# Kernel optimization log

Hardware: AMD Instinct MI355X
Metric: run time of the kernel (lower is better)

The kernel has to match this reference:

```python
import jax, jax.numpy as jnp
import numpy as np

EMB = 512
N_ROWS = 10000
N_PAIRS = 65536


def setup_inputs() -> dict:
    key = jax.random.key(0)
    ks = jax.random.split(key, 10)
    s1 = 1.0 / np.sqrt(2 * EMB)
    s2 = 1.0 / np.sqrt(128)
    s3 = 1.0 / np.sqrt(64)
    return {
        "pos_pairs": jax.random.randint(ks[0], (N_PAIRS, 3), 0, N_ROWS, dtype=jnp.int32),
        "neg_pairs": jax.random.randint(ks[1], (N_PAIRS, 3), 0, N_ROWS, dtype=jnp.int32),
        "drug_embedding": jax.random.normal(ks[2], (N_ROWS, EMB), dtype=jnp.float32),
        "target_embedding": jax.random.normal(ks[3], (N_ROWS, EMB), dtype=jnp.float32),
        "W1": jax.random.normal(ks[4], (2 * EMB, 128), dtype=jnp.float32) * s1,
        "b1": jnp.zeros((128,), dtype=jnp.float32),
        "W2": jax.random.normal(ks[5], (128, 64), dtype=jnp.float32) * s2,
        "b2": jnp.zeros((64,), dtype=jnp.float32),
        "W3": jax.random.normal(ks[6], (64, 1), dtype=jnp.float32) * s3,
        "b3": jnp.zeros((1,), dtype=jnp.float32),
    }


def _mlp(x, W1, b1, W2, b2, W3, b3):
    h = jax.nn.relu(x @ W1 + b1)
    h = jax.nn.relu(h @ W2 + b2)
    return (h @ W3 + b3)[..., 0]  # [N]


def _pair_loss(pairs, drug_emb, tgt_emb, W1, b1, W2, b2, W3, b3):
    d = drug_emb[pairs[:, 0]]            # [N, EMB]
    t1 = tgt_emb[pairs[:, 1]]            # [N, EMB]
    t2 = tgt_emb[pairs[:, 2]]            # [N, EMB]
    a1 = _mlp(jnp.concatenate([d, t1], axis=-1), W1, b1, W2, b2, W3, b3)
    a2 = _mlp(jnp.concatenate([d, t2], axis=-1), W1, b1, W2, b2, W3, b3)
    # per-pair MSE of scalar affinities = (a1 - a2)^2; mean over pairs
    return jnp.mean((a1 - a2) ** 2)


def reference(pos_pairs, neg_pairs, drug_embedding, target_embedding,
              W1, b1, W2, b2, W3, b3):
    pos = _pair_loss(pos_pairs, drug_embedding, target_embedding, W1, b1, W2, b2, W3, b3)
    neg = _pair_loss(neg_pairs, drug_embedding, target_embedding, W1, b1, W2, b2, W3, b3)
    return pos - neg
```

## Files before the change

### kernel.cpp

```cpp
#include <hip/hip_runtime.h>

#define EMB 512
#define NROWS 10000
#define NPAIRS 65536

typedef __bf16 bf16x8 __attribute__((ext_vector_type(8)));
typedef float  f32x4  __attribute__((ext_vector_type(4)));
typedef unsigned int u32x4 __attribute__((ext_vector_type(4)));

__device__ __forceinline__ void split2(float x0, float x1, unsigned* hw, unsigned* lw) {
    unsigned u0 = __float_as_uint(x0), u1 = __float_as_uint(x1);
    unsigned r0 = u0 + 0x7FFFu + ((u0 >> 16) & 1u);
    unsigned r1 = u1 + 0x7FFFu + ((u1 >> 16) & 1u);
    float h0 = __uint_as_float(r0 & 0xFFFF0000u);
    float h1 = __uint_as_float(r1 & 0xFFFF0000u);
    float l0 = x0 - h0, l1 = x1 - h1;
    unsigned v0 = __float_as_uint(l0), v1 = __float_as_uint(l1);
    unsigned s0 = v0 + 0x7FFFu + ((v0 >> 16) & 1u);
    unsigned s1 = v1 + 0x7FFFu + ((v1 >> 16) & 1u);
    *hw = (r0 >> 16) | (r1 & 0xFFFF0000u);
    *lw = (s0 >> 16) | (s1 & 0xFFFF0000u);
}

__global__ __launch_bounds__(256)
void k0_fragment(const float* __restrict__ W1, const float* __restrict__ W2,
                 unsigned short* __restrict__ W1Fhi, unsigned short* __restrict__ W1Flo,
                 unsigned short* __restrict__ W2Fhi, unsigned short* __restrict__ W2Flo)
{
    int e = blockIdx.x * 256 + threadIdx.x;
    float x;
    unsigned short *hp, *lp;
    if (e < 131072) {
        int i  = e & 7;
        int l  = (e >> 3) & 63;
        int nt = (e >> 9) & 7;
        int kt = (e >> 12) & 15;
        int t  = e >> 16;
        int k = kt * 32 + 8 * (l >> 4) + i;
        int n = nt * 16 + (l & 15);
        x = W1[(t * 512 + k) * 128 + n];
        hp = W1Fhi + e; lp = W1Flo + e;
    } else {
        int e2 = e - 131072;
        int i  = e2 & 7;
        int l  = (e2 >> 3) & 63;
        int nt = (e2 >> 9) & 3;
        int kt = e2 >> 11;
        int k = kt * 32 + 8 * (l >> 4) + i;
        int n = nt * 16 + (l & 15);
        x = W2[k * 64 + n];
        hp = W2Fhi + e2; lp = W2Flo + e2;
    }
    unsigned u = __float_as_uint(x);
    unsigned r = u + 0x7FFFu + ((u >> 16) & 1u);
    float hf = __uint_as_float(r & 0xFFFF0000u);
    float lf = x - hf;
    unsigned v = __float_as_uint(lf);
    unsigned s = v + 0x7FFFu + ((v >> 16) & 1u);
    *hp = (unsigned short)(r >> 16);
    *lp = (unsigned short)(s >> 16);
}

#define K1_TILES 625

__global__ __launch_bounds__(256)
void k1_pipe(const float* __restrict__ drug, const float* __restrict__ tgt,
             const unsigned* __restrict__ W1Fhi, const unsigned* __restrict__ W1Flo,
             const float* __restrict__ b1,
             float* __restrict__ D, float* __restrict__ T)
{
    __shared__ u32x4 Abuf[4][2][128];

    int bid = blockIdx.x, tid = threadIdx.x;
    bool isT = bid >= K1_TILES;
    int rt = isT ? bid - K1_TILES : bid;
    const float* emb = isT ? tgt : drug;
    float* out = isT ? T : D;
    int row0 = rt * 16;

    int wave = tid >> 6, lane = tid & 63;
    int g = lane >> 4, lm = lane & 15;
    int rr = lane >> 3, cc = lane & 7;
    int ntb = wave * 2;
    int rk = lm & 7;

    const u32x4* BH = (const u32x4*)W1Fhi + (isT ? 8192 : 0);
    const u32x4* BL = (const u32x4*)W1Flo + (isT ? 8192 : 0);

    const float* sp[2];
    #pragma unroll
    for (int it = 0; it < 2; it++) {
        int pr = it * 8 + rr;
        sp[it] = emb + (size_t)(row0 + pr) * EMB + ((cc ^ (pr & 7)) << 2);
    }

    f32x4 acc[2];
    #pragma unroll
    for (int j = 0; j < 2; j++) { acc[j][0]=0.f; acc[j][1]=0.f; acc[j][2]=0.f; acc[j][3]=0.f; }

    u32x4 bh0c = BH[(0 * 8 + ntb) * 64 + lane];
    u32x4 bh1c = BH[(0 * 8 + ntb + 1) * 64 + lane];
    u32x4 bl0c = BL[(0 * 8 + ntb) * 64 + lane];
    u32x4 bl1c = BL[(0 * 8 + ntb + 1) * 64 + lane];
    #pragma unroll
    for (int it = 0; it < 2; it++)
        __builtin_amdgcn_global_load_lds(
            (const __attribute__((address_space(1))) void*)(sp[it]),
            (__attribute__((address_space(3))) void*)((char*)&Abuf[wave][0][0] + it * 1024),
            16, 0, 0);

    #pragma unroll
    for (int kt = 0; kt < 16; kt++) {
        u32x4 bh0n, bh1n, bl0n, bl1n;
        if (kt < 15) {
            bh0n = BH[((kt + 1) * 8 + ntb) * 64 + lane];
            bh1n = BH[((kt + 1) * 8 + ntb + 1) * 64 + lane];
            bl0n = BL[((kt + 1) * 8 + ntb) * 64 + lane];
            bl1n = BL[((kt + 1) * 8 + ntb + 1) * 64 + lane];
            asm volatile("s_waitcnt lgkmcnt(0)" ::: "memory");
            #pragma unroll
            for (int it = 0; it < 2; it++)
                __builtin_amdgcn_global_load_lds(
                    (const __attribute__((address_space(1))) void*)(sp[it] + (kt + 1) * 32),
                    (__attribute__((address_space(3))) void*)((char*)&Abuf[wave][(kt + 1) & 1][0] + it * 1024),
                    16, 0, 0);
            asm volatile("s_waitcnt vmcnt(6)" ::: "memory");
        } else {
            asm volatile("s_waitcnt vmcnt(0)" ::: "memory");
        }
        const f32x4* Af = (const f32x4*)&Abuf[wave][kt & 1][0];
        f32x4 a0 = Af[lm * 8 + ((2 * g)     ^ rk)];
        f32x4 a1 = Af[lm * 8 + ((2 * g + 1) ^ rk)];
        unsigned h0, h1, h2, h3, l0, l1, l2, l3;
        split2(a0[0], a0[1], &h0, &l0);
        split2(a0[2], a0[3], &h1, &l1);
        split2(a1[0], a1[1], &h2, &l2);
        split2(a1[2], a1[3], &h3, &l3);
        u32x4 ah, al;
        ah[0]=h0; ah[1]=h1; ah[2]=h2; ah[3]=h3;
        al[0]=l0; al[1]=l1; al[2]=l2; al[3]=l3;
        bf16x8 Ah = __builtin_bit_cast(bf16x8, ah);
        bf16x8 Al = __builtin_bit_cast(bf16x8, al);
        bf16x8 Bh0 = __builtin_bit_cast(bf16x8, bh0c);
        bf16x8 Bh1 = __builtin_bit_cast(bf16x8, bh1c);
        bf16x8 Bl0 = __builtin_bit_cast(bf16x8, bl0c);
        bf16x8 Bl1 = __builtin_bit_cast(bf16x8, bl1c);
        acc[0] = __builtin_amdgcn_mfma_f32_16x16x32_bf16(Ah, Bh0, acc[0], 0, 0, 0);
        acc[1] = __builtin_amdgcn_mfma_f32_16x16x32_bf16(Ah, Bh1, acc[1], 0, 0, 0);
        acc[0] = __builtin_amdgcn_mfma_f32_16x16x32_bf16(Ah, Bl0, acc[0], 0, 0, 0);
        acc[1] = __builtin_amdgcn_mfma_f32_16x16x32_bf16(Ah, Bl1, acc[1], 0, 0, 0);
        acc[0] = __builtin_amdgcn_mfma_f32_16x16x32_bf16(Al, Bh0, acc[0], 0, 0, 0);
        acc[1] = __builtin_amdgcn_mfma_f32_16x16x32_bf16(Al, Bh1, acc[1], 0, 0, 0);
        bh0c = bh0n; bh1c = bh1n; bl0c = bl0n; bl1c = bl1n;
    }

    #pragma unroll
    for (int j = 0; j < 2; j++) {
        int col = (ntb + j) * 16 + lm;
        float bias = isT ? 0.f : b1[col];
        #pragma unroll
        for (int reg = 0; reg < 4; reg++) {
            int row = row0 + 4 * g + reg;
            out[row * 128 + col] = acc[j][reg] + bias;
        }
    }
}

__global__ __launch_bounds__(256)
void k2_pairs(const float* __restrict__ D, const float* __restrict__ T,
              const int* __restrict__ pos, const int* __restrict__ neg,
              const unsigned* __restrict__ W2Fhi, const unsigned* __restrict__ W2Flo,
              const float* __restrict__ b2, const float* __restrict__ W3,
              double* __restrict__ partials)
{
    __shared__ u32x4 Ash[4][768];

    int tid = threadIdx.x;
    int wave = tid >> 6, lane = tid & 63;
    int g = lane >> 4, lm = lane & 15;
    int rr = lane >> 3, cc = lane & 7;
    int gw = blockIdx.x * 4 + wave;
    const int* pairs = (gw < 2048) ? pos : neg;
    int p0 = (gw & 2047) * 32;

    const float* bp[12];
    #pragma unroll
    for (int it = 0; it < 12; it++) {
        int pr = it * 8 + rr;
        int idxv;
        const float* src;
        if (pr < 32) { idxv = pairs[(p0 + pr) * 3]; src = D; }
        else { int q = pr - 32; idxv = pairs[(p0 + (q >> 1)) * 3 + 1 + (q & 1)]; src = T; }
        bp[it] = src + (size_t)idxv * 128 + ((cc ^ (pr & 7)) << 2);
    }

    u32x4* A4w = &Ash[wave][0];
    const u32x4* BH4 = (const u32x4*)W2Fhi;
    const u32x4* BL4 = (const u32x4*)W2Flo;

    f32x4 acc[4][4];
    #pragma unroll
    for (int mt = 0; mt < 4; mt++)
        #pragma unroll
        for (int nt = 0; nt < 4; nt++) { acc[mt][nt][0]=0.f; acc[mt][nt][1]=0.f; acc[mt][nt][2]=0.f; acc[mt][nt][3]=0.f; }

    #pragma unroll 1
    for (int kt = 0; kt < 4; kt++) {
        u32x4 bh[4], bl[4];
        #pragma unroll
        for (int nt = 0; nt < 4; nt++) {
            bh[nt] = BH4[(kt * 4 + nt) * 64 + lane];
            bl[nt] = BL4[(kt * 4 + nt) * 64 + lane];
        }
        #pragma unroll
        for (int it = 0; it < 12; it++) {
            __builtin_amdgcn_global_load_lds(
                (const __attribute__((address_space(1))) void*)(bp[it] + kt * 32),
                (__attribute__((address_space(3))) void*)((char*)A4w + it * 1024),
                16, 0, 0);
        }
        asm volatile("s_waitcnt vmcnt(0)" ::: "memory");
        #pragma unroll
        for (int mt = 0; mt < 4; mt++) {
            int r = mt * 16 + lm;
            int p = r >> 1;
            int ds = p & 7, ts = r & 7;
            const f32x4* drow = (const f32x4*)(A4w + p * 8);
            const f32x4* trow = (const f32x4*)(A4w + (32 + r) * 8);
            f32x4 d0 = drow[(2 * g) ^ ds];
            f32x4 d1 = drow[(2 * g + 1) ^ ds];
            f32x4 t0 = trow[(2 * g) ^ ts];
            f32x4 t1 = trow[(2 * g + 1) ^ ts];
            float h0 = fmaxf(d0[0] + t0[0], 0.f), h1v = fmaxf(d0[1] + t0[1], 0.f);
            float h2 = fmaxf(d0[2] + t0[2], 0.f), h3 = fmaxf(d0[3] + t0[3], 0.f);
            float h4 = fmaxf(d1[0] + t1[0], 0.f), h5 = fmaxf(d1[1] + t1[1], 0.f);
            float h6 = fmaxf(d1[2] + t1[2], 0.f), h7 = fmaxf(d1[3] + t1[3], 0.f);
            unsigned hq0, hq1, hq2, hq3, lq0, lq1, lq2, lq3;
            split2(h0, h1v, &hq0, &lq0);
            split2(h2, h3,  &hq1, &lq1);
            split2(h4, h5,  &hq2, &lq2);
            split2(h6, h7,  &hq3, &lq3);
            u32x4 ah, al;
            ah[0]=hq0; ah[1]=hq1; ah[2]=hq2; ah[3]=hq3;
            al[0]=lq0; al[1]=lq1; al[2]=lq2; al[3]=lq3;
            bf16x8 Ahf = __builtin_bit_cast(bf16x8, ah);
            bf16x8 Alf = __builtin_bit_cast(bf16x8, al);
            #pragma unroll
            for (int nt = 0; nt < 4; nt++) {
                bf16x8 Bh = __builtin_bit_cast(bf16x8, bh[nt]);
                bf16x8 Bl = __builtin_bit_cast(bf16x8, bl[nt]);
                acc[mt][nt] = __builtin_amdgcn_mfma_f32_16x16x32_bf16(Ahf, Bh, acc[mt][nt], 0, 0, 0);
                acc[mt][nt] = __builtin_amdgcn_mfma_f32_16x16x32_bf16(Ahf, Bl, acc[mt][nt], 0, 0, 0);
                acc[mt][nt] = __builtin_amdgcn_mfma_f32_16x16x32_bf16(Alf, Bh, acc[mt][nt], 0, 0, 0);
            }
        }
        asm volatile("s_waitcnt lgkmcnt(0)" ::: "memory");
    }

    float b2v[4], w3v[4];
    #pragma unroll
    for (int nt = 0; nt < 4; nt++) { b2v[nt] = b2[nt * 16 + lm]; w3v[nt] = W3[nt * 16 + lm]; }

    float pr[4][4];
    #pragma unroll
    for (int mt = 0; mt < 4; mt++)
        #pragma unroll
        for (int reg = 0; reg < 4; reg++) {
            float s = 0.f;
            #pragma unroll
            for (int nt = 0; nt < 4; nt++) {
                float h2 = fmaxf(acc[mt][nt][reg] + b2v[nt], 0.f);
                s = fmaf(h2, w3v[nt], s);
            }
            pr[mt][reg] = s;
        }
    #pragma unroll
    for (int m = 1; m <= 8; m <<= 1)
        #pragma unroll
        for (int mt = 0; mt < 4; mt++)
            #pragma unroll
            for (int reg = 0; reg < 4; reg++)
                pr[mt][reg] += __shfl_xor(pr[mt][reg], m, 64);

    double dsq = 0.0;
    #pragma unroll
    for (int mt = 0; mt < 4; mt++) {
        float d0 = pr[mt][0] - pr[mt][1];
        float d1 = pr[mt][2] - pr[mt][3];
        dsq += (double)d0 * (double)d0 + (double)d1 * (double)d1;
    }
    dsq += __shfl_xor(dsq, 16, 64);
    dsq += __shfl_xor(dsq, 32, 64);

    __syncthreads();
    if (lane == 0) ((double*)&Ash[wave][0])[0] = dsq;
    __syncthreads();
    if (tid == 0) {
        double sum = 0.0;
        #pragma unroll
        for (int w = 0; w < 4; w++) sum += ((double*)&Ash[w][0])[0];
        partials[blockIdx.x] = sum;
    }
}

__global__ void k3_final(const double* __restrict__ partials, float* __restrict__ out)
{
    int lane = threadIdx.x;
    double sp = 0.0, sn = 0.0;
    #pragma unroll
    for (int i = 0; i < 8; i++) {
        sp += partials[lane + 64 * i];
        sn += partials[512 + lane + 64 * i];
    }
    #pragma unroll
    for (int m = 1; m <= 32; m <<= 1) {
        sp += __shfl_xor(sp, m, 64);
        sn += __shfl_xor(sn, m, 64);
    }
    if (lane == 0) out[0] = (float)((sp - sn) / (double)NPAIRS);
}

extern "C" void kernel_launch(void* const* d_in, const int* in_sizes, int n_in,
                              void* d_out, int out_size, void* d_ws, size_t ws_size,
                              hipStream_t stream) {
    const int*   pos  = (const int*)d_in[0];
    const int*   neg  = (const int*)d_in[1];
    const float* drug = (const float*)d_in[2];
    const float* tgt  = (const float*)d_in[3];
    const float* W1   = (const float*)d_in[4];
    const float* b1   = (const float*)d_in[5];
    const float* W2   = (const float*)d_in[6];
    const float* b2   = (const float*)d_in[7];
    const float* W3   = (const float*)d_in[8];

    float* Dp = (float*)d_ws;
    float* Tp = Dp + NROWS * 128;
    char* base = (char*)(Tp + NROWS * 128);
    unsigned short* W2Fhi = (unsigned short*)base;
    unsigned short* W2Flo = W2Fhi + 8192;
    unsigned short* W1Fhi = W2Flo + 8192;
    unsigned short* W1Flo = W1Fhi + 131072;
    double* partials = (double*)(W1Flo + 131072);
    float* out = (float*)d_out;

    k0_fragment<<<544, 256, 0, stream>>>(W1, W2, W1Fhi, W1Flo, W2Fhi, W2Flo);
    k1_pipe<<<2 * K1_TILES, 256, 0, stream>>>(drug, tgt, (const unsigned*)W1Fhi,
                                              (const unsigned*)W1Flo, b1, Dp, Tp);
    k2_pairs<<<1024, 256, 0, stream>>>(Dp, Tp, pos, neg, (const unsigned*)W2Fhi,
                                       (const unsigned*)W2Flo, b2, W3, partials);
    k3_final<<<1, 64, 0, stream>>>(partials, out);
}
```

Measured before the change: 59.86 us.

## Deepen k1 LDS prefetch to four stages and double-buffer k2 gathers

k1 now keeps three embedding tiles in flight through a 4-slot LDS ring instead of a 2-slot one, with vmcnt waits adjusted to match. k2 halves the pairs per wave (16 instead of 32), doubles the grid, and double-buffers both the gathered D/T rows in LDS and the W2 fragments in registers, so loads for the next k-step overlap the current MFMAs. k3 is updated to reduce the doubled number of partials. The aim is to hide global-load latency, at the cost of more LDS per block and less reuse of W2 fragments per wave.

```diff
diff --git a/kernel.cpp b/kernel.cpp
--- a/kernel.cpp
+++ b/kernel.cpp
@@ -64,12 +64,12 @@
 #define K1_TILES 625
 
 __global__ __launch_bounds__(256)
-void k1_pipe(const float* __restrict__ drug, const float* __restrict__ tgt,
-             const unsigned* __restrict__ W1Fhi, const unsigned* __restrict__ W1Flo,
-             const float* __restrict__ b1,
-             float* __restrict__ D, float* __restrict__ T)
+void k1_pipe4(const float* __restrict__ drug, const float* __restrict__ tgt,
+              const unsigned* __restrict__ W1Fhi, const unsigned* __restrict__ W1Flo,
+              const float* __restrict__ b1,
+              float* __restrict__ D, float* __restrict__ T)
 {
-    __shared__ u32x4 Abuf[4][2][128];
+    __shared__ u32x4 Abuf[4][4][128];
 
     int bid = blockIdx.x, tid = threadIdx.x;
     bool isT = bid >= K1_TILES;
@@ -103,11 +103,13 @@
     u32x4 bl0c = BL[(0 * 8 + ntb) * 64 + lane];
     u32x4 bl1c = BL[(0 * 8 + ntb + 1) * 64 + lane];
     #pragma unroll
-    for (int it = 0; it < 2; it++)
-        __builtin_amdgcn_global_load_lds(
-            (const __attribute__((address_space(1))) void*)(sp[it]),
-            (__attribute__((address_space(3))) void*)((char*)&Abuf[wave][0][0] + it * 1024),
-            16, 0, 0);
+    for (int s = 0; s < 3; s++)
+        #pragma unroll
+        for (int it = 0; it < 2; it++)
+            __builtin_amdgcn_global_load_lds(
+                (const __attribute__((address_space(1))) void*)(sp[it] + s * 32),
+                (__attribute__((address_space(3))) void*)((char*)&Abuf[wave][s][0] + it * 1024),
+                16, 0, 0);
 
     #pragma unroll
     for (int kt = 0; kt < 16; kt++) {
@@ -117,18 +119,24 @@
             bh1n = BH[((kt + 1) * 8 + ntb + 1) * 64 + lane];
             bl0n = BL[((kt + 1) * 8 + ntb) * 64 + lane];
             bl1n = BL[((kt + 1) * 8 + ntb + 1) * 64 + lane];
-            asm volatile("s_waitcnt lgkmcnt(0)" ::: "memory");
+        }
+        asm volatile("s_waitcnt lgkmcnt(0)" ::: "memory");
+        if (kt < 13) {
             #pragma unroll
             for (int it = 0; it < 2; it++)
                 __builtin_amdgcn_global_load_lds(
-                    (const __attribute__((address_space(1))) void*)(sp[it] + (kt + 1) * 32),
-                    (__attribute__((address_space(3))) void*)((char*)&Abuf[wave][(kt + 1) & 1][0] + it * 1024),
+                    (const __attribute__((address_space(1))) void*)(sp[it] + (kt + 3) * 32),
+                    (__attribute__((address_space(3))) void*)((char*)&Abuf[wave][(kt + 3) & 3][0] + it * 1024),
                     16, 0, 0);
+            asm volatile("s_waitcnt vmcnt(10)" ::: "memory");
+        } else if (kt == 13) {
+            asm volatile("s_waitcnt vmcnt(8)" ::: "memory");
+        } else if (kt == 14) {
             asm volatile("s_waitcnt vmcnt(6)" ::: "memory");
         } else {
             asm volatile("s_waitcnt vmcnt(0)" ::: "memory");
         }
-        const f32x4* Af = (const f32x4*)&Abuf[wave][kt & 1][0];
+        const f32x4* Af = (const f32x4*)&Abuf[wave][kt & 3][0];
         f32x4 a0 = Af[lm * 8 + ((2 * g)     ^ rk)];
         f32x4 a1 = Af[lm * 8 + ((2 * g + 1) ^ rk)];
         unsigned h0, h1, h2, h3, l0, l1, l2, l3;
@@ -173,60 +181,77 @@
               const float* __restrict__ b2, const float* __restrict__ W3,
               double* __restrict__ partials)
 {
-    __shared__ u32x4 Ash[4][768];
+    __shared__ u32x4 Ash[4][2][384];
 
     int tid = threadIdx.x;
     int wave = tid >> 6, lane = tid & 63;
     int g = lane >> 4, lm = lane & 15;
     int rr = lane >> 3, cc = lane & 7;
     int gw = blockIdx.x * 4 + wave;
-    const int* pairs = (gw < 2048) ? pos : neg;
-    int p0 = (gw & 2047) * 32;
-
-    const float* bp[12];
-    #pragma unroll
-    for (int it = 0; it < 12; it++) {
+    const int* pairs = (gw < 4096) ? pos : neg;
+    int p0 = (gw & 4095) * 16;
+
+    const float* bp[6];
+    #pragma unroll
+    for (int it = 0; it < 6; it++) {
         int pr = it * 8 + rr;
         int idxv;
         const float* src;
-        if (pr < 32) { idxv = pairs[(p0 + pr) * 3]; src = D; }
-        else { int q = pr - 32; idxv = pairs[(p0 + (q >> 1)) * 3 + 1 + (q & 1)]; src = T; }
+        if (pr < 16) { idxv = pairs[(p0 + pr) * 3]; src = D; }
+        else { int q = pr - 16; idxv = pairs[(p0 + (q >> 1)) * 3 + 1 + (q & 1)]; src = T; }
         bp[it] = src + (size_t)idxv * 128 + ((cc ^ (pr & 7)) << 2);
     }
 
-    u32x4* A4w = &Ash[wave][0];
     const u32x4* BH4 = (const u32x4*)W2Fhi;
     const u32x4* BL4 = (const u32x4*)W2Flo;
 
-    f32x4 acc[4][4];
-    #pragma unroll
-    for (int mt = 0; mt < 4; mt++)
+    f32x4 acc[2][4];
+    #pragma unroll
+    for (int mt = 0; mt < 2; mt++)
         #pragma unroll
         for (int nt = 0; nt < 4; nt++) { acc[mt][nt][0]=0.f; acc[mt][nt][1]=0.f; acc[mt][nt][2]=0.f; acc[mt][nt][3]=0.f; }
 
-    #pragma unroll 1
+    u32x4 bhc[4], blc[4];
+    #pragma unroll
+    for (int nt = 0; nt < 4; nt++) {
+        bhc[nt] = BH4[(0 * 4 + nt) * 64 + lane];
+        blc[nt] = BL4[(0 * 4 + nt) * 64 + lane];
+    }
+    #pragma unroll
+    for (int it = 0; it < 6; it++)
+        __builtin_amdgcn_global_load_lds(
+            (const __attribute__((address_space(1))) void*)(bp[it]),
+            (__attribute__((address_space(3))) void*)((char*)&Ash[wave][0][0] + it * 1024),
+            16, 0, 0);
+
+    #pragma unroll
     for (int kt = 0; kt < 4; kt++) {
-        u32x4 bh[4], bl[4];
-        #pragma unroll
-        for (int nt = 0; nt < 4; nt++) {
-            bh[nt] = BH4[(kt * 4 + nt) * 64 + lane];
-            bl[nt] = BL4[(kt * 4 + nt) * 64 + lane];
-        }
-        #pragma unroll
-        for (int it = 0; it < 12; it++) {
-            __builtin_amdgcn_global_load_lds(
-                (const __attribute__((address_space(1))) void*)(bp[it] + kt * 32),
-                (__attribute__((address_space(3))) void*)((char*)A4w + it * 1024),
-                16, 0, 0);
-        }
-        asm volatile("s_waitcnt vmcnt(0)" ::: "memory");
-        #pragma unroll
-        for (int mt = 0; mt < 4; mt++) {
+        u32x4 bhn[4], bln[4];
+        if (kt < 3) {
+            #pragma unroll
+            for (int nt = 0; nt < 4; nt++) {
+                bhn[nt] = BH4[((kt + 1) * 4 + nt) * 64 + lane];
+                bln[nt] = BL4[((kt + 1) * 4 + nt) * 64 + lane];
+            }
+            asm volatile("s_waitcnt lgkmcnt(0)" ::: "memory");
+            #pragma unroll
+            for (int it = 0; it < 6; it++)
+                __builtin_amdgcn_global_load_lds(
+                    (const __attribute__((address_space(1))) void*)(bp[it] + (kt + 1) * 32),
+                    (__attribute__((address_space(3))) void*)((char*)&Ash[wave][(kt + 1) & 1][0] + it * 1024),
+                    16, 0, 0);
+            asm volatile("s_waitcnt vmcnt(14)" ::: "memory");
+        } else {
+            asm volatile("s_waitcnt vmcnt(0)" ::: "memory");
+        }
+        const u32x4* A4w = &Ash[wave][kt & 1][0];
+        #pragma unroll
+        for (int mt = 0; mt < 2; mt++) {
             int r = mt * 16 + lm;
             int p = r >> 1;
             int ds = p & 7, ts = r & 7;
             const f32x4* drow = (const f32x4*)(A4w + p * 8);
-            const f32x4* trow = (const f32x4*)(A4w + (32 + r) * 8);
+            const f32x4* trow = (const f32x4*)(A4w + (16 + r) * 8);
             f32x4 d0 = drow[(2 * g) ^ ds];
             f32x4 d1 = drow[(2 * g + 1) ^ ds];
             f32x4 t0 = trow[(2 * g) ^ ts];
@@ -247,23 +272,24 @@
             bf16x8 Alf = __builtin_bit_cast(bf16x8, al);
             #pragma unroll
             for (int nt = 0; nt < 4; nt++) {
-                bf16x8 Bh = __builtin_bit_cast(bf16x8, bh[nt]);
-                bf16x8 Bl = __builtin_bit_cast(bf16x8, bl[nt]);
+                bf16x8 Bh = __builtin_bit_cast(bf16x8, bhc[nt]);
+                bf16x8 Bl = __builtin_bit_cast(bf16x8, blc[nt]);
                 acc[mt][nt] = __builtin_amdgcn_mfma_f32_16x16x32_bf16(Ahf, Bh, acc[mt][nt], 0, 0, 0);
                 acc[mt][nt] = __builtin_amdgcn_mfma_f32_16x16x32_bf16(Ahf, Bl, acc[mt][nt], 0, 0, 0);
                 acc[mt][nt] = __builtin_amdgcn_mfma_f32_16x16x32_bf16(Alf, Bh, acc[mt][nt], 0, 0, 0);
             }
         }
-        asm volatile("s_waitcnt lgkmcnt(0)" ::: "memory");
+        #pragma unroll
+        for (int nt = 0; nt < 4; nt++) { bhc[nt] = bhn[nt]; blc[nt] = bln[nt]; }
     }
 
     float b2v[4], w3v[4];
     #pragma unroll
     for (int nt = 0; nt < 4; nt++) { b2v[nt] = b2[nt * 16 + lm]; w3v[nt] = W3[nt * 16 + lm]; }
 
-    float pr[4][4];
-    #pragma unroll
-    for (int mt = 0; mt < 4; mt++)
+    float pr[2][4];
+    #pragma unroll
+    for (int mt = 0; mt < 2; mt++)
         #pragma unroll
         for (int reg = 0; reg < 4; reg++) {
             float s = 0.f;
@@ -277,14 +303,14 @@
     #pragma unroll
     for (int m = 1; m <= 8; m <<= 1)
         #pragma unroll
-        for (int mt = 0; mt < 4; mt++)
+        for (int mt = 0; mt < 2; mt++)
             #pragma unroll
             for (int reg = 0; reg < 4; reg++)
                 pr[mt][reg] += __shfl_xor(pr[mt][reg], m, 64);
 
     double dsq = 0.0;
     #pragma unroll
-    for (int mt = 0; mt < 4; mt++) {
+    for (int mt = 0; mt < 2; mt++) {
         float d0 = pr[mt][0] - pr[mt][1];
         float d1 = pr[mt][2] - pr[mt][3];
         dsq += (double)d0 * (double)d0 + (double)d1 * (double)d1;
@@ -293,12 +319,12 @@
     dsq += __shfl_xor(dsq, 32, 64);
 
     __syncthreads();
-    if (lane == 0) ((double*)&Ash[wave][0])[0] = dsq;
+    if (lane == 0) ((double*)&Ash[wave][0][0])[0] = dsq;
     __syncthreads();
     if (tid == 0) {
         double sum = 0.0;
         #pragma unroll
-        for (int w = 0; w < 4; w++) sum += ((double*)&Ash[w][0])[0];
+        for (int w = 0; w < 4; w++) sum += ((double*)&Ash[w][0][0])[0];
         partials[blockIdx.x] = sum;
     }
 }
@@ -308,9 +334,9 @@
     int lane = threadIdx.x;
     double sp = 0.0, sn = 0.0;
     #pragma unroll
-    for (int i = 0; i < 8; i++) {
+    for (int i = 0; i < 16; i++) {
         sp += partials[lane + 64 * i];
-        sn += partials[512 + lane + 64 * i];
+        sn += partials[1024 + lane + 64 * i];
     }
     #pragma unroll
     for (int m = 1; m <= 32; m <<= 1) {
@@ -344,9 +370,9 @@
     float* out = (float*)d_out;
 
     k0_fragment<<<544, 256, 0, stream>>>(W1, W2, W1Fhi, W1Flo, W2Fhi, W2Flo);
-    k1_pipe<<<2 * K1_TILES, 256, 0, stream>>>(drug, tgt, (const unsigned*)W1Fhi,
-                                              (const unsigned*)W1Flo, b1, Dp, Tp);
-    k2_pairs<<<1024, 256, 0, stream>>>(Dp, Tp, pos, neg, (const unsigned*)W2Fhi,
+    k1_pipe4<<<2 * K1_TILES, 256, 0, stream>>>(drug, tgt, (const unsigned*)W1Fhi,
+                                               (const unsigned*)W1Flo, b1, Dp, Tp);
+    k2_pairs<<<2048, 256, 0, stream>>>(Dp, Tp, pos, neg, (const unsigned*)W2Fhi,
                                        (const unsigned*)W2Flo, b2, W3, partials);
     k3_final<<<1, 64, 0, stream>>>(partials, out);
 }
```

Measured after the change: 57.36 us. 4.2% less time.
